# Kernel optimization log

Measured on AMD Instinct MI355X. Metric: run time of the kernel, lower is better.

Reference implementation:

```python
import jax, jax.numpy as jnp
import numpy as np

N_X = 32640   # total xlmr subword tokens (64 seqs x 510 tokens)
N_S = 16320   # total stanza word tokens (2 subwords per word)
E = 65280     # dependency edges (bidirectional, avg degree ~4)
D = 768
GCN_DIM = 256
GCN_NUM = 2
POS_DIM = 4
N_UPOS = 17
N_LABEL = 5


def setup_inputs() -> dict:
    key = jax.random.key(0)
    ks = jax.random.split(key, 8)
    x = jax.random.normal(ks[0], (N_X, D), dtype=jnp.float32)
    # mapStanza2Xlmr as segment ids: xlmr token j belongs to stanza word j//2
    seg = jnp.arange(N_X, dtype=jnp.int32) // 2
    edge_index = jax.random.randint(ks[1], (2, E), 0, N_S, dtype=jnp.int32)
    upos_ids = jax.random.randint(ks[2], (N_S,), 0, N_UPOS, dtype=jnp.int32)
    Wc = jax.random.normal(ks[3], (D, GCN_DIM), dtype=jnp.float32) * 0.02
    bc = jnp.zeros((GCN_DIM,), dtype=jnp.float32)
    gcn_W = jax.random.normal(ks[4], (GCN_NUM, GCN_DIM, GCN_DIM), dtype=jnp.float32) * 0.05
    gcn_b = jnp.zeros((GCN_NUM, GCN_DIM), dtype=jnp.float32)
    upos_table = jax.random.normal(ks[5], (N_UPOS, POS_DIM), dtype=jnp.float32)
    Wcls = jax.random.normal(ks[6], (D + GCN_DIM + POS_DIM, N_LABEL), dtype=jnp.float32) * 0.02
    bcls = jnp.zeros((N_LABEL,), dtype=jnp.float32)
    return {"x": x, "seg": seg, "edge_index": edge_index, "upos_ids": upos_ids,
            "Wc": Wc, "bc": bc, "gcn_W": gcn_W, "gcn_b": gcn_b,
            "upos_table": upos_table, "Wcls": Wcls, "bcls": bcls}


def _gcn_conv(h, srcs, dsts, W, b, n):
    # PyG GCNConv: h' = D^-1/2 (A+I) D^-1/2 (h W) + b  (self loops already in srcs/dsts)
    h = h @ W
    deg = jax.ops.segment_sum(jnp.ones_like(dsts, h.dtype), dsts, num_segments=n)
    dinv = jax.lax.rsqrt(deg)  # deg >= 1 because of self loops
    coef = dinv[srcs] * dinv[dsts]
    out = jax.ops.segment_sum(h[srcs] * coef[:, None], dsts, num_segments=n)
    return out + b


def reference(x, seg, edge_index, upos_ids, Wc, bc, gcn_W, gcn_b, upos_table, Wcls, bcls):
    # mapStanza2Xlmr: mean-pool subword embeddings into stanza word embeddings
    cnt = jax.ops.segment_sum(jnp.ones((N_X,), x.dtype), seg, num_segments=N_S)
    stanza = jax.ops.segment_sum(x, seg, num_segments=N_S) / cnt[:, None]  # [N_S, D]
    # GCN over dependency edges (gcn_mode=0: biedges)
    h = stanza @ Wc + bc
    self_idx = jnp.arange(N_S, dtype=edge_index.dtype)
    srcs = jnp.concatenate([edge_index[0], self_idx])
    dsts = jnp.concatenate([edge_index[1], self_idx])
    for i in range(GCN_NUM):
        h = jax.nn.relu(_gcn_conv(h, srcs, dsts, gcn_W[i], gcn_b[i], N_S))
    # POS embedding + concat + relu
    pos = upos_table[upos_ids]                                  # [N_S, POS_DIM]
    info = jax.nn.relu(jnp.concatenate([h, pos], axis=1))       # [N_S, GCN_DIM+POS_DIM]
    # mapXlmr2Stanza: each subword gathers its (single) word's info
    append = info[seg]                                          # [N_X, GCN_DIM+POS_DIM]
    tok = jnp.concatenate([x, append], axis=1)                  # [N_X, 1028]
    logits = jax.nn.relu(tok) @ Wcls + bcls
    return jax.nn.log_softmax(logits, axis=1)
```

## Files before the change

### kernel.cpp

```cpp
#include <hip/hip_runtime.h>

#define NXT 32640
#define NS  16320
#define NE  65280
#define DD  768
#define GD  256
#define NLAB 5
#define CAP 32

typedef __attribute__((ext_vector_type(8))) short bf16x8;
typedef __attribute__((ext_vector_type(8))) unsigned short u16x8;
typedef __attribute__((ext_vector_type(4))) float f32x4;
typedef __attribute__((ext_vector_type(8))) float f32x8;

__device__ inline unsigned short f2b(float f) {
    unsigned int u = __float_as_uint(f);
    unsigned int r = (u + 0x7FFFu + ((u >> 16) & 1u)) >> 16;
    return (unsigned short)r;
}
__device__ inline float b2f(unsigned short h) {
    return __uint_as_float((unsigned int)h << 16);
}

__device__ inline void tile_transpose(const float* __restrict__ src, unsigned short* __restrict__ dst,
                                      int K, int k0, int n0, int tid) {
    __shared__ unsigned short tl[64][65];
#pragma unroll
    for (int i = 0; i < 16; ++i) {
        int idx = tid + i * 256;
        int r = idx >> 6, c = idx & 63;
        tl[r][c] = f2b(src[(size_t)(k0 + r) * GD + n0 + c]);
    }
    __syncthreads();
#pragma unroll
    for (int i = 0; i < 16; ++i) {
        int idx = tid + i * 256;
        int rr = idx >> 6, cc = idx & 63;
        dst[(size_t)(n0 + rr) * K + k0 + cc] = tl[cc][rr];
    }
}

__global__ void k_setup(int* __restrict__ cnt,
                        const float* __restrict__ Wc, unsigned short* __restrict__ WcT,
                        const float* __restrict__ gcn_W, unsigned short* __restrict__ WT,
                        const float* __restrict__ Wcls, float* __restrict__ WclsT,
                        const float* __restrict__ upos_table, const float* __restrict__ bcls,
                        float* __restrict__ posLogit) {
    int b = blockIdx.x, t = threadIdx.x;
    if (b < 64) {
        int i = b * 256 + t;
        if (i < NS) cnt[i] = 0;
    } else if (b < 112) {
        int tile = b - 64;
        tile_transpose(Wc, WcT, DD, (tile >> 2) * 64, (tile & 3) * 64, t);
    } else if (b < 128) {
        int tile = b - 112;
        tile_transpose(gcn_W, WT, GD, (tile >> 2) * 64, (tile & 3) * 64, t);
    } else if (b < 144) {
        int tile = b - 128;
        tile_transpose(gcn_W + (size_t)GD * GD, WT + (size_t)GD * GD, GD,
                       (tile >> 2) * 64, (tile & 3) * 64, t);
    } else if (b < 159) {
        int idx = (b - 144) * 256 + t;
        if (idx < NLAB * DD) {
            int l = idx / DD, k = idx - l * DD;
            WclsT[idx] = Wcls[(size_t)k * NLAB + l];
        }
    } else {
        if (t < 17 * NLAB) {
            int u = t / NLAB, l = t - u * NLAB;
            float a = bcls[l];
#pragma unroll
            for (int p = 0; p < 4; ++p) {
                float pv = upos_table[u * 4 + p];
                pv = pv > 0.f ? pv : 0.f;
                a += pv * Wcls[(size_t)(DD + GD + p) * NLAB + l];
            }
            posLogit[t] = a;
        }
    }
}

__global__ __launch_bounds__(512, 2) void k_mega0(const float* __restrict__ x,
                                                  const unsigned short* __restrict__ WcT,
                                                  const float* __restrict__ WclsT,
                                                  const float* __restrict__ bc,
                                                  const int* __restrict__ ei,
                                                  int* __restrict__ cnt, int* __restrict__ csr_src,
                                                  unsigned short* __restrict__ h_bf,
                                                  float* __restrict__ partial) {
    __shared__ unsigned short lds[1536 * 8];
    const int tid = threadIdx.x;
    if (blockIdx.x >= 512) {
        int e = (blockIdx.x - 512) * 512 + tid;
        if (e < NE) {
            int dst = ei[NE + e];
            int slot = atomicAdd(&cnt[dst], 1);
            if (slot < CAP) csr_src[(size_t)dst * CAP + slot] = ei[e];
        }
        return;
    }
    const int xcd = blockIdx.x & 7, slot = blockIdx.x >> 3;
    const int bm64 = (slot >> 1) * 8 + xcd;
    const int bn   = slot & 1;
    if (bm64 >= 255) return;
    const int bm = bm64 * 64;

    const int lane = tid & 63;
    const int wv   = tid >> 6;
    const int wr   = wv & 3, wc = wv >> 2;

    const int kc = tid & 7, rl = (tid >> 3) & 15, g = tid >> 7;
    const int w_loc = g * 16 + rl;
    const float* xr0 = x + (size_t)(2 * (bm + w_loc)) * DD + kc * 8;
    const float* xr1 = xr0 + DD;
    const int aw_slot = (kc >> 2) * 256 + g * 64 + (kc & 3) * 16 + rl;
    const float* wcl = WclsT + kc * 8;

    const unsigned short* srcB[2];
#pragma unroll
    for (int q = 0; q < 2; ++q) {
        int s = q * 512 + tid;
        int gran = s >> 8, chunk = s & 255;
        int nh = gran >> 1, kh = gran & 1;
        int rg = chunk >> 6, kc2 = (chunk >> 4) & 3, rl2 = chunk & 15;
        srcB[q] = WcT + (size_t)(bn * 128 + nh * 64 + rg * 16 + rl2) * DD + kh * 32 + kc2 * 8;
    }

    const bf16x8* ldsv = (const bf16x8*)lds;
    f32x4 acc[4] = {};
    float lg0[NLAB] = {}, lg1[NLAB] = {};

    for (int it = 0; it < 12; ++it) {
        const int k0 = it * 64;
#pragma unroll
        for (int q = 0; q < 2; ++q)
            __builtin_amdgcn_global_load_lds(srcB[q] + k0, lds + (size_t)(512 + q * 512 + tid) * 8, 16, 0, 0);
        f32x8 va = *(const f32x8*)(xr0 + k0);
        f32x8 vb = *(const f32x8*)(xr1 + k0);
        u16x8 pool;
#pragma unroll
        for (int i = 0; i < 8; ++i) pool[i] = f2b((va[i] + vb[i]) * 0.5f);
        *(u16x8*)(lds + (size_t)aw_slot * 8) = pool;
        if (bn == 0) {
#pragma unroll
            for (int l = 0; l < NLAB; ++l) {
                f32x8 wv8 = *(const f32x8*)(wcl + (size_t)l * DD + k0);
#pragma unroll
                for (int i = 0; i < 8; ++i) {
                    float ra = va[i] > 0.f ? va[i] : 0.f;
                    float rb = vb[i] > 0.f ? vb[i] : 0.f;
                    lg0[l] += ra * wv8[i];
                    lg1[l] += rb * wv8[i];
                }
            }
        }
        __syncthreads();
#pragma unroll
        for (int kh = 0; kh < 2; ++kh) {
            bf16x8 a = ldsv[kh * 256 + wr * 64 + lane];
#pragma unroll
            for (int n = 0; n < 4; ++n) {
                bf16x8 b = ldsv[512 + (wc * 2 + kh) * 256 + n * 64 + lane];
                acc[n] = __builtin_amdgcn_mfma_f32_16x16x32_bf16(a, b, acc[n], 0, 0, 0);
            }
        }
        __syncthreads();
    }

    const int rl2 = lane & 15, rq = lane >> 4;
    {
        int row0 = bm + wr * 16 + rq * 4;
#pragma unroll
        for (int n = 0; n < 4; ++n) {
            int col = bn * 128 + wc * 64 + n * 16 + rl2;
            float bv = bc[col];
#pragma unroll
            for (int r = 0; r < 4; ++r)
                h_bf[(size_t)(row0 + r) * GD + col] = f2b(acc[n][r] + bv);
        }
    }

    if (bn == 0) {
#pragma unroll
        for (int l = 0; l < NLAB; ++l) {
            lg0[l] += __shfl_xor(lg0[l], 1); lg0[l] += __shfl_xor(lg0[l], 2); lg0[l] += __shfl_xor(lg0[l], 4);
            lg1[l] += __shfl_xor(lg1[l], 1); lg1[l] += __shfl_xor(lg1[l], 2); lg1[l] += __shfl_xor(lg1[l], 4);
        }
        if (kc == 0) {
            int w = bm + w_loc;
            float* pp = partial + (size_t)w * 2 * NLAB;
#pragma unroll
            for (int l = 0; l < NLAB; ++l) { pp[l] = lg0[l]; pp[NLAB + l] = lg1[l]; }
        }
    }
}

__global__ __launch_bounds__(256) void k_gemm(const unsigned short* __restrict__ A,
                                              const unsigned short* __restrict__ BT,
                                              const float* __restrict__ bias,
                                              unsigned short* __restrict__ out,
                                              int K, int nbn) {
    __shared__ unsigned short lds[1536 * 8];
    const int tid  = threadIdx.x;
    const int lane = tid & 63;
    const int wv   = tid >> 6;
    const int wr   = wv >> 1, wc = wv & 1;
    const int bm   = (blockIdx.x / nbn) * 64;
    const int bn   = (blockIdx.x % nbn) * 128;

    const int g  = tid >> 6, w_ = tid & 63, kc = w_ >> 4, rl = w_ & 15;
    const unsigned short* srcA  = A  + (size_t)(bm + g * 16 + rl) * K + kc * 8;
    const unsigned short* srcB0 = BT + (size_t)(bn      + g * 16 + rl) * K + kc * 8;
    const unsigned short* srcB1 = BT + (size_t)(bn + 64 + g * 16 + rl) * K + kc * 8;

    unsigned short* dA0 = lds + (size_t)tid * 8;
    unsigned short* dA1 = dA0 + 256 * 8;
    unsigned short* dB  = lds + (size_t)(512 + tid) * 8;

    const bf16x8* fA = (const bf16x8*)lds + (wr * 2) * 64 + lane;
    const bf16x8* fB = (const bf16x8*)lds + 512 + wc * 256 + lane;

    f32x4 acc[2][4] = {};
    for (int k0 = 0; k0 < K; k0 += 64) {
        __builtin_amdgcn_global_load_lds(srcA  + k0,      dA0,            16, 0, 0);
        __builtin_amdgcn_global_load_lds(srcA  + k0 + 32, dA1,            16, 0, 0);
        __builtin_amdgcn_global_load_lds(srcB0 + k0,      dB,             16, 0, 0);
        __builtin_amdgcn_global_load_lds(srcB1 + k0,      dB + 256 * 8,   16, 0, 0);
        __builtin_amdgcn_global_load_lds(srcB0 + k0 + 32, dB + 512 * 8,   16, 0, 0);
        __builtin_amdgcn_global_load_lds(srcB1 + k0 + 32, dB + 768 * 8,   16, 0, 0);
        __syncthreads();
#pragma unroll
        for (int kh = 0; kh < 2; ++kh) {
            bf16x8 a0 = fA[kh * 256], a1 = fA[kh * 256 + 64];
            const bf16x8* fb = fB + kh * 512;
            bf16x8 b0 = fb[0], b1 = fb[64], b2 = fb[128], b3 = fb[192];
            acc[0][0] = __builtin_amdgcn_mfma_f32_16x16x32_bf16(a0, b0, acc[0][0], 0, 0, 0);
            acc[0][1] = __builtin_amdgcn_mfma_f32_16x16x32_bf16(a0, b1, acc[0][1], 0, 0, 0);
            acc[0][2] = __builtin_amdgcn_mfma_f32_16x16x32_bf16(a0, b2, acc[0][2], 0, 0, 0);
            acc[0][3] = __builtin_amdgcn_mfma_f32_16x16x32_bf16(a0, b3, acc[0][3], 0, 0, 0);
            acc[1][0] = __builtin_amdgcn_mfma_f32_16x16x32_bf16(a1, b0, acc[1][0], 0, 0, 0);
            acc[1][1] = __builtin_amdgcn_mfma_f32_16x16x32_bf16(a1, b1, acc[1][1], 0, 0, 0);
            acc[1][2] = __builtin_amdgcn_mfma_f32_16x16x32_bf16(a1, b2, acc[1][2], 0, 0, 0);
            acc[1][3] = __builtin_amdgcn_mfma_f32_16x16x32_bf16(a1, b3, acc[1][3], 0, 0, 0);
        }
        __syncthreads();
    }

    const int rl2 = lane & 15, rq = lane >> 4;
#pragma unroll
    for (int m = 0; m < 2; ++m) {
        int row0 = bm + wr * 32 + m * 16 + rq * 4;
#pragma unroll
        for (int n = 0; n < 4; ++n) {
            int col = bn + wc * 64 + n * 16 + rl2;
            float bv = bias ? bias[col] : 0.f;
#pragma unroll
            for (int r = 0; r < 4; ++r)
                out[(size_t)(row0 + r) * GD + col] = f2b(acc[m][n][r] + bv);
        }
    }
}

__global__ void k_gather(const int* __restrict__ cnt, const int* __restrict__ csr_src,
                         const unsigned short* __restrict__ hW,
                         const float* __restrict__ b, unsigned short* __restrict__ hout) {
    int w    = blockIdx.x * 4 + (threadIdx.x >> 6);
    int lane = threadIdx.x & 63;
    int c = cnt[w];
    float dw = rsqrtf((float)c + 1.0f);
    const int* sl = csr_src + (size_t)w * CAP;
    float ax = 0.f, ay = 0.f, az = 0.f, aw = 0.f;
    for (int j = 0; j < c; ++j) {
        int src = sl[j];
        float cf = rsqrtf((float)cnt[src] + 1.0f) * dw;
        ushort4 v = *(const ushort4*)&hW[(size_t)src * GD + lane * 4];
        ax += cf * b2f(v.x); ay += cf * b2f(v.y); az += cf * b2f(v.z); aw += cf * b2f(v.w);
    }
    ushort4 sv = *(const ushort4*)&hW[(size_t)w * GD + lane * 4];
    f32x4 bv = *(const f32x4*)&b[lane * 4];
    float c2 = dw * dw;
    float rx = ax + b2f(sv.x) * c2 + bv[0];
    float ry = ay + b2f(sv.y) * c2 + bv[1];
    float rz = az + b2f(sv.z) * c2 + bv[2];
    float rw = aw + b2f(sv.w) * c2 + bv[3];
    ushort4 o;
    o.x = f2b(rx > 0.f ? rx : 0.f);
    o.y = f2b(ry > 0.f ? ry : 0.f);
    o.z = f2b(rz > 0.f ? rz : 0.f);
    o.w = f2b(rw > 0.f ? rw : 0.f);
    *(ushort4*)&hout[(size_t)w * GD + lane * 4] = o;
}

__global__ void k_gather_final(const int* __restrict__ cnt, const int* __restrict__ csr_src,
                               const unsigned short* __restrict__ hW,
                               const float* __restrict__ b,
                               const float* __restrict__ partial,
                               const int* __restrict__ upos_ids,
                               const float* __restrict__ posLogit,
                               const float* __restrict__ Wcls,
                               float* __restrict__ out) {
    int w    = blockIdx.x * 4 + (threadIdx.x >> 6);
    int lane = threadIdx.x & 63;
    int c = cnt[w];
    float dw = rsqrtf((float)c + 1.0f);
    const int* sl = csr_src + (size_t)w * CAP;
    float ax = 0.f, ay = 0.f, az = 0.f, aw = 0.f;
    for (int j = 0; j < c; ++j) {
        int src = sl[j];
        float cf = rsqrtf((float)cnt[src] + 1.0f) * dw;
        ushort4 v = *(const ushort4*)&hW[(size_t)src * GD + lane * 4];
        ax += cf * b2f(v.x); ay += cf * b2f(v.y); az += cf * b2f(v.z); aw += cf * b2f(v.w);
    }
    ushort4 sv = *(const ushort4*)&hW[(size_t)w * GD + lane * 4];
    f32x4 bv = *(const f32x4*)&b[lane * 4];
    float c2 = dw * dw;
    float hv[4];
    hv[0] = ax + b2f(sv.x) * c2 + bv[0];
    hv[1] = ay + b2f(sv.y) * c2 + bv[1];
    hv[2] = az + b2f(sv.z) * c2 + bv[2];
    hv[3] = aw + b2f(sv.w) * c2 + bv[3];
    float acc[NLAB] = {};
#pragma unroll
    for (int i = 0; i < 4; ++i) {
        float v = hv[i] > 0.f ? hv[i] : 0.f;
        const float* wr = Wcls + (size_t)(DD + lane * 4 + i) * NLAB;
#pragma unroll
        for (int l = 0; l < NLAB; ++l) acc[l] += v * wr[l];
    }
#pragma unroll
    for (int off = 32; off > 0; off >>= 1)
#pragma unroll
        for (int l = 0; l < NLAB; ++l) acc[l] += __shfl_xor(acc[l], off);
    if (lane == 0) {
        const float* pl = posLogit + (size_t)upos_ids[w] * NLAB;
        const float* pp = partial + (size_t)w * 2 * NLAB;
#pragma unroll
        for (int t = 0; t < 2; ++t) {
            float lg[NLAB];
#pragma unroll
            for (int l = 0; l < NLAB; ++l) lg[l] = acc[l] + pp[t * NLAB + l] + pl[l];
            float m = lg[0];
#pragma unroll
            for (int l = 1; l < NLAB; ++l) m = fmaxf(m, lg[l]);
            float s = 0.f;
#pragma unroll
            for (int l = 0; l < NLAB; ++l) s += __expf(lg[l] - m);
            float lse = __logf(s) + m;
            float* op = out + (size_t)(2 * w + t) * NLAB;
#pragma unroll
            for (int l = 0; l < NLAB; ++l) op[l] = lg[l] - lse;
        }
    }
}

extern "C" void kernel_launch(void* const* d_in, const int* in_sizes, int n_in,
                              void* d_out, int out_size, void* d_ws, size_t ws_size,
                              hipStream_t stream) {
    const float* x          = (const float*)d_in[0];
    const int*   ei         = (const int*)d_in[2];
    const int*   upos_ids   = (const int*)d_in[3];
    const float* Wc         = (const float*)d_in[4];
    const float* bc         = (const float*)d_in[5];
    const float* gcn_W      = (const float*)d_in[6];
    const float* gcn_b      = (const float*)d_in[7];
    const float* upos_table = (const float*)d_in[8];
    const float* Wcls       = (const float*)d_in[9];
    const float* bcls       = (const float*)d_in[10];
    float* out = (float*)d_out;

    char* ws = (char*)d_ws;
    float* partial          = (float*)ws;            ws += (size_t)NXT * NLAB * 4;
    float* WclsT            = (float*)ws;            ws += (size_t)NLAB * DD * 4;
    float* posLogit         = (float*)ws;            ws += (size_t)17 * NLAB * 4;
    unsigned short* h_bf    = (unsigned short*)ws;   ws += (size_t)NS * GD * 2;
    unsigned short* hW_bf   = (unsigned short*)ws;   ws += (size_t)NS * GD * 2;
    unsigned short* WcT     = (unsigned short*)ws;   ws += (size_t)DD * GD * 2;
    unsigned short* WT      = (unsigned short*)ws;   ws += (size_t)2 * GD * GD * 2;
    int* cnt                = (int*)ws;              ws += (size_t)NS * 4;
    int* csr_src            = (int*)ws;              ws += (size_t)NS * CAP * 4;

    k_setup<<<160, 256, 0, stream>>>(cnt, Wc, WcT, gcn_W, WT, Wcls, WclsT,
                                     upos_table, bcls, posLogit);
    k_mega0<<<640, 512, 0, stream>>>(x, WcT, WclsT, bc, ei, cnt, csr_src, h_bf, partial);
    k_gemm<<<(NS / 64) * 2, 256, 0, stream>>>(h_bf, WT, nullptr, hW_bf, GD, 2);
    k_gather<<<NS / 4, 256, 0, stream>>>(cnt, csr_src, hW_bf, gcn_b, h_bf);
    k_gemm<<<(NS / 64) * 2, 256, 0, stream>>>(h_bf, WT + (size_t)GD * GD, nullptr, hW_bf, GD, 2);
    k_gather_final<<<NS / 4, 256, 0, stream>>>(cnt, csr_src, hW_bf, gcn_b + GD,
                                               partial, upos_ids, posLogit, Wcls, out);
}
```

Measured before the change: 115.0 us.

## Fuse GCN GEMMs and gathers into one cooperative persistent kernel

Replaces the four GCN launches (two GEMMs, two gathers) with a single cooperative kernel of 510 blocks that runs each layer's GEMM and then its neighbor gather, separated by grid-wide syncs. Each block computes one 64x128 GEMM tile and then gathers 32 nodes. This removes per-launch overhead and the tail gaps between dependent kernels. In exchange it relies on all 510 blocks being co-resident, which the launch bounds of 2 blocks per CU are meant to allow, and it adds grid.sync costs.

```diff
diff --git a/kernel.cpp b/kernel.cpp
--- a/kernel.cpp
+++ b/kernel.cpp
@@ -1,4 +1,7 @@
 #include <hip/hip_runtime.h>
+#include <hip/hip_cooperative_groups.h>
+
+namespace cg = cooperative_groups;
 
 #define NXT 32640
 #define NS  16320
@@ -196,160 +199,163 @@
     }
 }
 
-__global__ __launch_bounds__(256) void k_gemm(const unsigned short* __restrict__ A,
-                                              const unsigned short* __restrict__ BT,
-                                              const float* __restrict__ bias,
-                                              unsigned short* __restrict__ out,
-                                              int K, int nbn) {
+__global__ __launch_bounds__(256, 2) void k_gcn(const int* __restrict__ cnt,
+                                                const int* __restrict__ csr_src,
+                                                unsigned short* __restrict__ h_bf,
+                                                unsigned short* __restrict__ hW_bf,
+                                                const unsigned short* __restrict__ WT,
+                                                const float* __restrict__ gcn_b,
+                                                const float* __restrict__ partial,
+                                                const int* __restrict__ upos_ids,
+                                                const float* __restrict__ posLogit,
+                                                const float* __restrict__ Wcls,
+                                                float* __restrict__ out) {
+    cg::grid_group grid = cg::this_grid();
     __shared__ unsigned short lds[1536 * 8];
     const int tid  = threadIdx.x;
     const int lane = tid & 63;
-    const int wv   = tid >> 6;
-    const int wr   = wv >> 1, wc = wv & 1;
-    const int bm   = (blockIdx.x / nbn) * 64;
-    const int bn   = (blockIdx.x % nbn) * 128;
-
+    const int wvv  = tid >> 6;
+
+    const int wr = wvv >> 1, wcc = wvv & 1;
+    const int bm = (blockIdx.x >> 1) * 64;
+    const int bn = (blockIdx.x & 1) * 128;
     const int g  = tid >> 6, w_ = tid & 63, kc = w_ >> 4, rl = w_ & 15;
-    const unsigned short* srcA  = A  + (size_t)(bm + g * 16 + rl) * K + kc * 8;
-    const unsigned short* srcB0 = BT + (size_t)(bn      + g * 16 + rl) * K + kc * 8;
-    const unsigned short* srcB1 = BT + (size_t)(bn + 64 + g * 16 + rl) * K + kc * 8;
-
+    const size_t offA  = (size_t)(bm + g * 16 + rl) * GD + kc * 8;
+    const size_t offB0 = (size_t)(bn      + g * 16 + rl) * GD + kc * 8;
+    const size_t offB1 = (size_t)(bn + 64 + g * 16 + rl) * GD + kc * 8;
     unsigned short* dA0 = lds + (size_t)tid * 8;
     unsigned short* dA1 = dA0 + 256 * 8;
     unsigned short* dB  = lds + (size_t)(512 + tid) * 8;
-
     const bf16x8* fA = (const bf16x8*)lds + (wr * 2) * 64 + lane;
-    const bf16x8* fB = (const bf16x8*)lds + 512 + wc * 256 + lane;
-
-    f32x4 acc[2][4] = {};
-    for (int k0 = 0; k0 < K; k0 += 64) {
-        __builtin_amdgcn_global_load_lds(srcA  + k0,      dA0,            16, 0, 0);
-        __builtin_amdgcn_global_load_lds(srcA  + k0 + 32, dA1,            16, 0, 0);
-        __builtin_amdgcn_global_load_lds(srcB0 + k0,      dB,             16, 0, 0);
-        __builtin_amdgcn_global_load_lds(srcB1 + k0,      dB + 256 * 8,   16, 0, 0);
-        __builtin_amdgcn_global_load_lds(srcB0 + k0 + 32, dB + 512 * 8,   16, 0, 0);
-        __builtin_amdgcn_global_load_lds(srcB1 + k0 + 32, dB + 768 * 8,   16, 0, 0);
-        __syncthreads();
-#pragma unroll
-        for (int kh = 0; kh < 2; ++kh) {
-            bf16x8 a0 = fA[kh * 256], a1 = fA[kh * 256 + 64];
-            const bf16x8* fb = fB + kh * 512;
-            bf16x8 b0 = fb[0], b1 = fb[64], b2 = fb[128], b3 = fb[192];
-            acc[0][0] = __builtin_amdgcn_mfma_f32_16x16x32_bf16(a0, b0, acc[0][0], 0, 0, 0);
-            acc[0][1] = __builtin_amdgcn_mfma_f32_16x16x32_bf16(a0, b1, acc[0][1], 0, 0, 0);
-            acc[0][2] = __builtin_amdgcn_mfma_f32_16x16x32_bf16(a0, b2, acc[0][2], 0, 0, 0);
-            acc[0][3] = __builtin_amdgcn_mfma_f32_16x16x32_bf16(a0, b3, acc[0][3], 0, 0, 0);
-            acc[1][0] = __builtin_amdgcn_mfma_f32_16x16x32_bf16(a1, b0, acc[1][0], 0, 0, 0);
-            acc[1][1] = __builtin_amdgcn_mfma_f32_16x16x32_bf16(a1, b1, acc[1][1], 0, 0, 0);
-            acc[1][2] = __builtin_amdgcn_mfma_f32_16x16x32_bf16(a1, b2, acc[1][2], 0, 0, 0);
-            acc[1][3] = __builtin_amdgcn_mfma_f32_16x16x32_bf16(a1, b3, acc[1][3], 0, 0, 0);
-        }
-        __syncthreads();
-    }
-
+    const bf16x8* fB = (const bf16x8*)lds + 512 + wcc * 256 + lane;
     const int rl2 = lane & 15, rq = lane >> 4;
-#pragma unroll
-    for (int m = 0; m < 2; ++m) {
-        int row0 = bm + wr * 32 + m * 16 + rq * 4;
-#pragma unroll
-        for (int n = 0; n < 4; ++n) {
-            int col = bn + wc * 64 + n * 16 + rl2;
-            float bv = bias ? bias[col] : 0.f;
-#pragma unroll
-            for (int r = 0; r < 4; ++r)
-                out[(size_t)(row0 + r) * GD + col] = f2b(acc[m][n][r] + bv);
-        }
-    }
-}
-
-__global__ void k_gather(const int* __restrict__ cnt, const int* __restrict__ csr_src,
-                         const unsigned short* __restrict__ hW,
-                         const float* __restrict__ b, unsigned short* __restrict__ hout) {
-    int w    = blockIdx.x * 4 + (threadIdx.x >> 6);
-    int lane = threadIdx.x & 63;
-    int c = cnt[w];
-    float dw = rsqrtf((float)c + 1.0f);
-    const int* sl = csr_src + (size_t)w * CAP;
-    float ax = 0.f, ay = 0.f, az = 0.f, aw = 0.f;
-    for (int j = 0; j < c; ++j) {
-        int src = sl[j];
-        float cf = rsqrtf((float)cnt[src] + 1.0f) * dw;
-        ushort4 v = *(const ushort4*)&hW[(size_t)src * GD + lane * 4];
-        ax += cf * b2f(v.x); ay += cf * b2f(v.y); az += cf * b2f(v.z); aw += cf * b2f(v.w);
-    }
-    ushort4 sv = *(const ushort4*)&hW[(size_t)w * GD + lane * 4];
-    f32x4 bv = *(const f32x4*)&b[lane * 4];
-    float c2 = dw * dw;
-    float rx = ax + b2f(sv.x) * c2 + bv[0];
-    float ry = ay + b2f(sv.y) * c2 + bv[1];
-    float rz = az + b2f(sv.z) * c2 + bv[2];
-    float rw = aw + b2f(sv.w) * c2 + bv[3];
-    ushort4 o;
-    o.x = f2b(rx > 0.f ? rx : 0.f);
-    o.y = f2b(ry > 0.f ? ry : 0.f);
-    o.z = f2b(rz > 0.f ? rz : 0.f);
-    o.w = f2b(rw > 0.f ? rw : 0.f);
-    *(ushort4*)&hout[(size_t)w * GD + lane * 4] = o;
-}
-
-__global__ void k_gather_final(const int* __restrict__ cnt, const int* __restrict__ csr_src,
-                               const unsigned short* __restrict__ hW,
-                               const float* __restrict__ b,
-                               const float* __restrict__ partial,
-                               const int* __restrict__ upos_ids,
-                               const float* __restrict__ posLogit,
-                               const float* __restrict__ Wcls,
-                               float* __restrict__ out) {
-    int w    = blockIdx.x * 4 + (threadIdx.x >> 6);
-    int lane = threadIdx.x & 63;
-    int c = cnt[w];
-    float dw = rsqrtf((float)c + 1.0f);
-    const int* sl = csr_src + (size_t)w * CAP;
-    float ax = 0.f, ay = 0.f, az = 0.f, aw = 0.f;
-    for (int j = 0; j < c; ++j) {
-        int src = sl[j];
-        float cf = rsqrtf((float)cnt[src] + 1.0f) * dw;
-        ushort4 v = *(const ushort4*)&hW[(size_t)src * GD + lane * 4];
-        ax += cf * b2f(v.x); ay += cf * b2f(v.y); az += cf * b2f(v.z); aw += cf * b2f(v.w);
-    }
-    ushort4 sv = *(const ushort4*)&hW[(size_t)w * GD + lane * 4];
-    f32x4 bv = *(const f32x4*)&b[lane * 4];
-    float c2 = dw * dw;
-    float hv[4];
-    hv[0] = ax + b2f(sv.x) * c2 + bv[0];
-    hv[1] = ay + b2f(sv.y) * c2 + bv[1];
-    hv[2] = az + b2f(sv.z) * c2 + bv[2];
-    hv[3] = aw + b2f(sv.w) * c2 + bv[3];
-    float acc[NLAB] = {};
-#pragma unroll
-    for (int i = 0; i < 4; ++i) {
-        float v = hv[i] > 0.f ? hv[i] : 0.f;
-        const float* wr = Wcls + (size_t)(DD + lane * 4 + i) * NLAB;
-#pragma unroll
-        for (int l = 0; l < NLAB; ++l) acc[l] += v * wr[l];
-    }
-#pragma unroll
-    for (int off = 32; off > 0; off >>= 1)
-#pragma unroll
-        for (int l = 0; l < NLAB; ++l) acc[l] += __shfl_xor(acc[l], off);
-    if (lane == 0) {
-        const float* pl = posLogit + (size_t)upos_ids[w] * NLAB;
-        const float* pp = partial + (size_t)w * 2 * NLAB;
-#pragma unroll
-        for (int t = 0; t < 2; ++t) {
-            float lg[NLAB];
-#pragma unroll
-            for (int l = 0; l < NLAB; ++l) lg[l] = acc[l] + pp[t * NLAB + l] + pl[l];
-            float m = lg[0];
-#pragma unroll
-            for (int l = 1; l < NLAB; ++l) m = fmaxf(m, lg[l]);
-            float s = 0.f;
-#pragma unroll
-            for (int l = 0; l < NLAB; ++l) s += __expf(lg[l] - m);
-            float lse = __logf(s) + m;
-            float* op = out + (size_t)(2 * w + t) * NLAB;
-#pragma unroll
-            for (int l = 0; l < NLAB; ++l) op[l] = lg[l] - lse;
+
+#pragma unroll
+    for (int layer = 0; layer < 2; ++layer) {
+        const unsigned short* A  = h_bf;
+        const unsigned short* BT = WT + (size_t)layer * GD * GD;
+        f32x4 acc[2][4] = {};
+        for (int k0 = 0; k0 < GD; k0 += 64) {
+            __builtin_amdgcn_global_load_lds(A + offA + k0,       dA0,          16, 0, 0);
+            __builtin_amdgcn_global_load_lds(A + offA + k0 + 32,  dA1,          16, 0, 0);
+            __builtin_amdgcn_global_load_lds(BT + offB0 + k0,     dB,           16, 0, 0);
+            __builtin_amdgcn_global_load_lds(BT + offB1 + k0,     dB + 256 * 8, 16, 0, 0);
+            __builtin_amdgcn_global_load_lds(BT + offB0 + k0 + 32, dB + 512 * 8, 16, 0, 0);
+            __builtin_amdgcn_global_load_lds(BT + offB1 + k0 + 32, dB + 768 * 8, 16, 0, 0);
+            __syncthreads();
+#pragma unroll
+            for (int kh = 0; kh < 2; ++kh) {
+                bf16x8 a0 = fA[kh * 256], a1 = fA[kh * 256 + 64];
+                const bf16x8* fb = fB + kh * 512;
+                bf16x8 b0 = fb[0], b1 = fb[64], b2 = fb[128], b3 = fb[192];
+                acc[0][0] = __builtin_amdgcn_mfma_f32_16x16x32_bf16(a0, b0, acc[0][0], 0, 0, 0);
+                acc[0][1] = __builtin_amdgcn_mfma_f32_16x16x32_bf16(a0, b1, acc[0][1], 0, 0, 0);
+                acc[0][2] = __builtin_amdgcn_mfma_f32_16x16x32_bf16(a0, b2, acc[0][2], 0, 0, 0);
+                acc[0][3] = __builtin_amdgcn_mfma_f32_16x16x32_bf16(a0, b3, acc[0][3], 0, 0, 0);
+                acc[1][0] = __builtin_amdgcn_mfma_f32_16x16x32_bf16(a1, b0, acc[1][0], 0, 0, 0);
+                acc[1][1] = __builtin_amdgcn_mfma_f32_16x16x32_bf16(a1, b1, acc[1][1], 0, 0, 0);
+                acc[1][2] = __builtin_amdgcn_mfma_f32_16x16x32_bf16(a1, b2, acc[1][2], 0, 0, 0);
+                acc[1][3] = __builtin_amdgcn_mfma_f32_16x16x32_bf16(a1, b3, acc[1][3], 0, 0, 0);
+            }
+            __syncthreads();
+        }
+#pragma unroll
+        for (int m = 0; m < 2; ++m) {
+            int row0 = bm + wr * 32 + m * 16 + rq * 4;
+#pragma unroll
+            for (int n = 0; n < 4; ++n) {
+                int col = bn + wcc * 64 + n * 16 + rl2;
+#pragma unroll
+                for (int r = 0; r < 4; ++r)
+                    hW_bf[(size_t)(row0 + r) * GD + col] = f2b(acc[m][n][r]);
+            }
+        }
+        grid.sync();
+
+        const float* bvec = gcn_b + (size_t)layer * GD;
+        int wbase = blockIdx.x * 32 + wvv * 8;
+        if (layer == 0) {
+            for (int wi = 0; wi < 8; ++wi) {
+                int w = wbase + wi;
+                int c = cnt[w];
+                float dw = rsqrtf((float)c + 1.0f);
+                const int* sl = csr_src + (size_t)w * CAP;
+                float ax = 0.f, ay = 0.f, az = 0.f, aw = 0.f;
+                for (int j = 0; j < c; ++j) {
+                    int src = sl[j];
+                    float cf = rsqrtf((float)cnt[src] + 1.0f) * dw;
+                    ushort4 v = *(const ushort4*)&hW_bf[(size_t)src * GD + lane * 4];
+                    ax += cf * b2f(v.x); ay += cf * b2f(v.y); az += cf * b2f(v.z); aw += cf * b2f(v.w);
+                }
+                ushort4 sv = *(const ushort4*)&hW_bf[(size_t)w * GD + lane * 4];
+                f32x4 bv = *(const f32x4*)&bvec[lane * 4];
+                float c2 = dw * dw;
+                float rx = ax + b2f(sv.x) * c2 + bv[0];
+                float ry = ay + b2f(sv.y) * c2 + bv[1];
+                float rz = az + b2f(sv.z) * c2 + bv[2];
+                float rw = aw + b2f(sv.w) * c2 + bv[3];
+                ushort4 o;
+                o.x = f2b(rx > 0.f ? rx : 0.f);
+                o.y = f2b(ry > 0.f ? ry : 0.f);
+                o.z = f2b(rz > 0.f ? rz : 0.f);
+                o.w = f2b(rw > 0.f ? rw : 0.f);
+                *(ushort4*)&h_bf[(size_t)w * GD + lane * 4] = o;
+            }
+            grid.sync();
+        } else {
+            for (int wi = 0; wi < 8; ++wi) {
+                int w = wbase + wi;
+                int c = cnt[w];
+                float dw = rsqrtf((float)c + 1.0f);
+                const int* sl = csr_src + (size_t)w * CAP;
+                float ax = 0.f, ay = 0.f, az = 0.f, aw = 0.f;
+                for (int j = 0; j < c; ++j) {
+                    int src = sl[j];
+                    float cf = rsqrtf((float)cnt[src] + 1.0f) * dw;
+                    ushort4 v = *(const ushort4*)&hW_bf[(size_t)src * GD + lane * 4];
+                    ax += cf * b2f(v.x); ay += cf * b2f(v.y); az += cf * b2f(v.z); aw += cf * b2f(v.w);
+                }
+                ushort4 sv = *(const ushort4*)&hW_bf[(size_t)w * GD + lane * 4];
+                f32x4 bv = *(const f32x4*)&bvec[lane * 4];
+                float c2 = dw * dw;
+                float hv[4];
+                hv[0] = ax + b2f(sv.x) * c2 + bv[0];
+                hv[1] = ay + b2f(sv.y) * c2 + bv[1];
+                hv[2] = az + b2f(sv.z) * c2 + bv[2];
+                hv[3] = aw + b2f(sv.w) * c2 + bv[3];
+                float accl[NLAB] = {};
+#pragma unroll
+                for (int i = 0; i < 4; ++i) {
+                    float v = hv[i] > 0.f ? hv[i] : 0.f;
+                    const float* wrow = Wcls + (size_t)(DD + lane * 4 + i) * NLAB;
+#pragma unroll
+                    for (int l = 0; l < NLAB; ++l) accl[l] += v * wrow[l];
+                }
+#pragma unroll
+                for (int off = 32; off > 0; off >>= 1)
+#pragma unroll
+                    for (int l = 0; l < NLAB; ++l) accl[l] += __shfl_xor(accl[l], off);
+                if (lane == 0) {
+                    const float* pl = posLogit + (size_t)upos_ids[w] * NLAB;
+                    const float* pp = partial + (size_t)w * 2 * NLAB;
+#pragma unroll
+                    for (int t = 0; t < 2; ++t) {
+                        float lg[NLAB];
+#pragma unroll
+                        for (int l = 0; l < NLAB; ++l) lg[l] = accl[l] + pp[t * NLAB + l] + pl[l];
+                        float m = lg[0];
+#pragma unroll
+                        for (int l = 1; l < NLAB; ++l) m = fmaxf(m, lg[l]);
+                        float s = 0.f;
+#pragma unroll
+                        for (int l = 0; l < NLAB; ++l) s += __expf(lg[l] - m);
+                        float lse = __logf(s) + m;
+                        float* op = out + (size_t)(2 * w + t) * NLAB;
+#pragma unroll
+                        for (int l = 0; l < NLAB; ++l) op[l] = lg[l] - lse;
+                    }
+                }
+            }
         }
     }
 }
@@ -383,9 +389,10 @@
     k_setup<<<160, 256, 0, stream>>>(cnt, Wc, WcT, gcn_W, WT, Wcls, WclsT,
                                      upos_table, bcls, posLogit);
     k_mega0<<<640, 512, 0, stream>>>(x, WcT, WclsT, bc, ei, cnt, csr_src, h_bf, partial);
-    k_gemm<<<(NS / 64) * 2, 256, 0, stream>>>(h_bf, WT, nullptr, hW_bf, GD, 2);
-    k_gather<<<NS / 4, 256, 0, stream>>>(cnt, csr_src, hW_bf, gcn_b, h_bf);
-    k_gemm<<<(NS / 64) * 2, 256, 0, stream>>>(h_bf, WT + (size_t)GD * GD, nullptr, hW_bf, GD, 2);
-    k_gather_final<<<NS / 4, 256, 0, stream>>>(cnt, csr_src, hW_bf, gcn_b + GD,
-                                               partial, upos_ids, posLogit, Wcls, out);
-}
+    {
+        void* args[] = {(void*)&cnt, (void*)&csr_src, (void*)&h_bf, (void*)&hW_bf,
+                        (void*)&WT, (void*)&gcn_b, (void*)&partial, (void*)&upos_ids,
+                        (void*)&posLogit, (void*)&Wcls, (void*)&out};
+        hipLaunchCooperativeKernel((void*)k_gcn, dim3(510), dim3(256), args, 0, stream);
+    }
+}
```

New measurement: 341.9 us. 2.97x slower.
